# Performance work log

Hardware: AMD Instinct MI355X
Metric: run time of the kernel (lower is better)

## Reference

```python
import jax, jax.numpy as jnp
import numpy as np

D_MODEL, D_K, D_V, NUM_HEADS = 1024, 64, 64, 16
B, T = 4, 2048


def setup_inputs() -> dict:
    key = jax.random.key(0)
    ks = jax.random.split(key, 9)
    s = 0.02
    inp = {
        "input_Q": jax.random.normal(ks[0], (B, T, D_MODEL), dtype=jnp.float32),
        # causal mask: True = masked out (matches torch masked_fill semantics)
        "mask": jnp.triu(jnp.ones((T, T), dtype=bool), k=1),
        "Wq": jax.random.normal(ks[1], (D_MODEL, D_K * NUM_HEADS), dtype=jnp.float32) * s,
        "bq": jnp.zeros((D_K * NUM_HEADS,), dtype=jnp.float32),
        "Wk": jax.random.normal(ks[2], (D_MODEL, D_K * NUM_HEADS), dtype=jnp.float32) * s,
        "bk": jnp.zeros((D_K * NUM_HEADS,), dtype=jnp.float32),
        "Wv": jax.random.normal(ks[3], (D_MODEL, D_V * NUM_HEADS), dtype=jnp.float32) * s,
        "bv": jnp.zeros((D_V * NUM_HEADS,), dtype=jnp.float32),
        "Wo": jax.random.normal(ks[4], (D_V * NUM_HEADS, D_MODEL), dtype=jnp.float32) * s,
        "bo": jnp.zeros((D_MODEL,), dtype=jnp.float32),
    }
    return inp


def reference(input_Q, mask, Wq, bq, Wk, bk, Wv, bv, Wo, bo):
    b, t, _ = input_Q.shape
    h, dk, dv = NUM_HEADS, D_K, D_V
    # projections, then split heads: [b, t, h*d] -> [b, h, t, d]
    Q = (input_Q @ Wq + bq).reshape(b, t, h, dk).transpose(0, 2, 1, 3)
    K = (input_Q @ Wk + bk).reshape(b, t, h, dk).transpose(0, 2, 1, 3)
    V = (input_Q @ Wv + bv).reshape(b, t, h, dv).transpose(0, 2, 1, 3)
    # scaled dot-product attention with full [b, h, t, t] scores (as original)
    scores = jnp.einsum("bhqd,bhkd->bhqk", Q, K) * (1.0 / np.sqrt(dk).astype(np.float32))
    scores = jnp.where(mask, jnp.float32(-jnp.inf), scores)
    attn = jax.nn.softmax(scores, axis=-1)
    ctx = jnp.einsum("bhqk,bhkd->bhqd", attn, V)  # [b, h, t, dv]
    combined = ctx.transpose(0, 2, 1, 3).reshape(b, t, h * dv)
    return combined @ Wo + bo
```

## Files before the change

kernel.cpp:

```cpp
#include <hip/hip_runtime.h>
#include <hip/hip_bf16.h>
#include <stdint.h>

#define B_  4
#define T_  2048
#define H_  16
#define DH  64
#define DM  1024

typedef unsigned short u16;
typedef float  f32x4  __attribute__((ext_vector_type(4)));
typedef u16    u16x4  __attribute__((ext_vector_type(4)));
typedef __bf16 bf16x8 __attribute__((ext_vector_type(8)));
typedef bf16x8 __attribute__((may_alias, aligned(16))) bf16x8_a;
typedef u16x4  __attribute__((may_alias, aligned(8)))  u16x4_a;

__device__ __forceinline__ void gld16(void* lds, const void* g) {
  __builtin_amdgcn_global_load_lds((const __attribute__((address_space(1))) unsigned int*)g,
                                   (__attribute__((address_space(3))) unsigned int*)lds,
                                   16, 0, 0);
}
__device__ __forceinline__ u16 f2b(float f) {
  __bf16 h = (__bf16)f; return __builtin_bit_cast(unsigned short, h);
}

__global__ void prep(const float* __restrict__ X,
                     const float* __restrict__ Wq, const float* __restrict__ Wk,
                     const float* __restrict__ Wv, const float* __restrict__ Wo,
                     u16* __restrict__ Xb,
                     u16* __restrict__ WqT, u16* __restrict__ WkT,
                     u16* __restrict__ WvT, u16* __restrict__ WoT) {
  if (blockIdx.z == 4) {
    const int bi = blockIdx.y * 16 + blockIdx.x;
#pragma unroll
    for (int p = 0; p < 32; ++p) {
      const int i = bi * 32768 + p * 1024 + threadIdx.x * 4;
      const f32x4 v = *(const f32x4*)&X[i];
      u16x4 o;
      o.x = f2b(v.x); o.y = f2b(v.y); o.z = f2b(v.z); o.w = f2b(v.w);
      *(u16x4_a*)&Xb[i] = o;
    }
    return;
  }
  const float* in; u16* out;
  switch (blockIdx.z) {
    case 0: in = Wq; out = WqT; break;
    case 1: in = Wk; out = WkT; break;
    case 2: in = Wv; out = WvT; break;
    default: in = Wo; out = WoT; break;
  }
  __shared__ u16 t[64][65];
  const int bx = blockIdx.x * 64, by = blockIdx.y * 64;
  const int tx = threadIdx.x & 63, ty = threadIdx.x >> 6;
  for (int i = ty; i < 64; i += 4) t[i][tx] = f2b(in[(size_t)(by + i) * DM + bx + tx]);
  __syncthreads();
  for (int i = ty; i < 64; i += 4) out[(size_t)(bx + i) * DM + by + tx] = t[tx][i];
}

__device__ __forceinline__ void gemm_bt_128(
    const u16* __restrict__ A, const u16* __restrict__ BT,
    const float* __restrict__ bias, float oscale,
    u16* __restrict__ C, float* __restrict__ Cf, int mode)
{
  constexpr int K = 1024, N = 1024;
  __shared__ __attribute__((aligned(16))) u16 lAB[128 * 128];
  u16* lA = lAB;
  u16* lB = lAB + 128 * 64;
  const int tid  = threadIdx.x;
  const int lane = tid & 63;
  const int quad = lane >> 4, ln = lane & 15;
  const int ln7 = ln & 7;
  const int wave = tid >> 6;
  const int wm = wave >> 1, wn = wave & 1;
  const int m0 = blockIdx.y * 128, n0 = blockIdx.x * 128;

  const f32x4 fz = {0.f, 0.f, 0.f, 0.f};
  f32x4 acc[4][4];
#pragma unroll
  for (int i = 0; i < 4; i++)
#pragma unroll
    for (int j = 0; j < 4; j++) acc[i][j] = fz;

  for (int k0 = 0; k0 < K; k0 += 64) {
    __syncthreads();
#pragma unroll
    for (int p = 0; p < 4; ++p) {
      const int P = p * 256 + tid;
      const int row = P >> 3, c = (P & 7) ^ (row & 7);
      gld16(&lA[P * 8], &A [(size_t)(m0 + row) * K + k0 + c * 8]);
      gld16(&lB[P * 8], &BT[(size_t)(n0 + row) * K + k0 + c * 8]);
    }
    __syncthreads();
#pragma unroll
    for (int ks = 0; ks < 2; ++ks) {
      bf16x8 af[4], bf[4];
#pragma unroll
      for (int i = 0; i < 4; i++)
        af[i] = *(const bf16x8_a*)&lA[(wm * 64 + i * 16 + ln) * 64 + (((ks * 4 + quad) ^ ln7) << 3)];
#pragma unroll
      for (int j = 0; j < 4; j++)
        bf[j] = *(const bf16x8_a*)&lB[(wn * 64 + j * 16 + ln) * 64 + (((ks * 4 + quad) ^ ln7) << 3)];
#pragma unroll
      for (int i = 0; i < 4; i++)
#pragma unroll
        for (int j = 0; j < 4; j++)
          acc[i][j] = __builtin_amdgcn_mfma_f32_16x16x32_bf16(af[i], bf[j], acc[i][j], 0, 0, 0);
    }
  }

  if (mode == 1) {
    __syncthreads();
#pragma unroll
    for (int j = 0; j < 4; j++) {
      const int nl = wn * 64 + j * 16 + ln;
      const float bn = bias[n0 + nl];
#pragma unroll
      for (int i = 0; i < 4; i++) {
        const int ml = wm * 64 + i * 16 + quad * 4;
        u16x4 o;
#pragma unroll
        for (int r = 0; r < 4; r++) o[r] = f2b((acc[i][j][r] + bn) * oscale);
        const int sc = (ml >> 3) ^ (nl & 15);
        *(u16x4_a*)&lAB[nl * 128 + sc * 8 + (ml & 7)] = o;
      }
    }
    __syncthreads();
    const int bb = m0 >> 11, t0 = m0 & 2047;
#pragma unroll
    for (int it = 0; it < 8; ++it) {
      const int P = it * 256 + tid;
      const int nl = P >> 4, c = P & 15;
      const bf16x8 v = *(const bf16x8_a*)&lAB[nl * 128 + ((c ^ (nl & 15)) << 3)];
      const int n = n0 + nl, h = n >> 6, d = n & 63;
      *(bf16x8_a*)&C[((size_t)((bb * H_ + h) * DH + d)) * T_ + t0 + c * 8] = v;
    }
    return;
  }

#pragma unroll
  for (int j = 0; j < 4; j++) {
    const int n = n0 + wn * 64 + j * 16 + ln;
    const float bn = bias[n];
#pragma unroll
    for (int i = 0; i < 4; i++) {
      const int mb = m0 + wm * 64 + i * 16 + quad * 4;
#pragma unroll
      for (int r = 0; r < 4; r++) {
        const int m = mb + r;
        const float v = (acc[i][j][r] + bn) * oscale;
        if (mode == 0) {
          const int b = m >> 11, t = m & 2047, h = n >> 6, d = n & 63;
          C[((size_t)((b * H_ + h) * T_ + t)) * DH + d] = f2b(v);
        } else {
          Cf[(size_t)m * N + n] = v;
        }
      }
    }
  }
}

__global__ __launch_bounds__(256, 2) void qkv_gemm(
    const u16* __restrict__ X,
    const u16* __restrict__ WqT, const u16* __restrict__ WkT, const u16* __restrict__ WvT,
    const float* __restrict__ bq, const float* __restrict__ bk, const float* __restrict__ bv,
    u16* __restrict__ Qo, u16* __restrict__ Ko, u16* __restrict__ Vto)
{
  const u16 *BT; const float* bias; u16* C; float sc; int mode;
  if (blockIdx.z == 0)      { BT = WqT; bias = bq; C = Qo;  sc = 0.1803368801111144f; mode = 0; }
  else if (blockIdx.z == 1) { BT = WkT; bias = bk; C = Ko;  sc = 1.0f;                mode = 0; }
  else                      { BT = WvT; bias = bv; C = Vto; sc = 1.0f;                mode = 1; }
  gemm_bt_128(X, BT, bias, sc, C, nullptr, mode);
}

__global__ __launch_bounds__(256, 2) void out_gemm(
    const u16* __restrict__ ctx, const u16* __restrict__ WoT,
    const float* __restrict__ bo, float* __restrict__ out)
{
  gemm_bt_128(ctx, WoT, bo, 1.0f, nullptr, out, 2);
}

__global__ __launch_bounds__(512, 4) void flash_attn(
    const u16* __restrict__ Q, const u16* __restrict__ Kg,
    const u16* __restrict__ Vt, u16* __restrict__ ctx)
{
  __shared__ __attribute__((aligned(16))) u16 lK[2][128 * 64];
  __shared__ __attribute__((aligned(16))) u16 lV[2][64 * 128];
  __shared__ __attribute__((aligned(16))) u16 lP[128 * 64];

  const int bh = blockIdx.x;
  const int b  = bh >> 4, h = bh & 15;
  const int qi = 15 - blockIdx.y;
  const int q0 = qi * 128;
  const int tid = threadIdx.x;
  const int lane = tid & 63, wave = tid >> 6;
  const int quad = lane >> 4, ln = lane & 15;
  const int ln7 = ln & 7, ln8 = ln >> 3;
  const int w16 = wave * 16;

  const u16* Qbh = Q  + (size_t)bh * T_ * DH;
  const u16* Kbh = Kg + (size_t)bh * T_ * DH;
  const u16* Vbh = Vt + (size_t)bh * DH * T_;

  auto stage_kv = [&](int kt, int bufw) {
    const int t0 = kt << 7;
    u16* dK = lK[bufw]; u16* dV = lV[bufw];
#pragma unroll
    for (int p = 0; p < 2; ++p) {
      const int P = p * 512 + tid;
      const int row = P >> 3, c = (P & 7) ^ (row & 7);
      gld16(&dK[P * 8], &Kbh[(size_t)(t0 + row) * DH + c * 8]);
    }
#pragma unroll
    for (int p = 0; p < 2; ++p) {
      const int P = p * 512 + tid;
      const int row = P >> 4, c = (P & 15) ^ (row & 15);
      gld16(&dV[P * 8], &Vbh[(size_t)row * T_ + t0 + c * 8]);
    }
  };

#pragma unroll
  for (int p = 0; p < 2; ++p) {
    const int P = p * 512 + tid;
    const int row = P >> 3, c = (P & 7) ^ (row & 7);
    gld16(&lP[P * 8], &Qbh[(size_t)(q0 + row) * DH + c * 8]);
  }
  stage_kv(0, 0);
  asm volatile("s_waitcnt vmcnt(4)" ::: "memory");
  __builtin_amdgcn_s_barrier();
  bf16x8 aq[2];
#pragma unroll
  for (int ks = 0; ks < 2; ++ks)
    aq[ks] = *(const bf16x8_a*)&lP[(w16 + ln) * 64 + (((ks * 4 + quad) ^ ln7) << 3)];

  bf16x8 ones;
#pragma unroll
  for (int i = 0; i < 8; i++) ones[i] = (__bf16)1.0f;

  const f32x4 fz = {0.f, 0.f, 0.f, 0.f};
  f32x4 accO[4];
  f32x4 accL;
#pragma unroll
  for (int j = 0; j < 4; j++) accO[j] = fz;
  accL = fz;

  auto compute_tile = [&](int kt, const u16* lKb, const u16* lVb, bool MASK) {
    const int t0 = kt * 128;
#pragma unroll
    for (int half = 0; half < 2; ++half) {
      f32x4 s[4];
#pragma unroll
      for (int jj = 0; jj < 4; jj++) s[jj] = fz;
      __builtin_amdgcn_s_setprio(1);
#pragma unroll
      for (int ks = 0; ks < 2; ++ks) {
        bf16x8 bk4[4];
#pragma unroll
        for (int jj = 0; jj < 4; jj++)
          bk4[jj] = *(const bf16x8_a*)&lKb[((half * 4 + jj) * 16 + ln) * 64 + (((ks * 4 + quad) ^ ln7) << 3)];
#pragma unroll
        for (int jj = 0; jj < 4; jj++)
          s[jj] = __builtin_amdgcn_mfma_f32_16x16x32_bf16(aq[ks], bk4[jj], s[jj], 0, 0, 0);
      }
      __builtin_amdgcn_s_setprio(0);

#pragma unroll
      for (int jj = 0; jj < 4; jj++)
#pragma unroll
        for (int r = 0; r < 4; r++) {
          float z = s[jj][r];
          if (MASK) {
            const int qrow = q0 + w16 + quad * 4 + r;
            if ((t0 + (half * 4 + jj) * 16 + ln) > qrow) z = -INFINITY;
          }
          s[jj][r] = __builtin_amdgcn_exp2f(z);
        }

#pragma unroll
      for (int jj = 0; jj < 4; jj++) {
        const int c = jj * 2 + ln8;
#pragma unroll
        for (int r = 0; r < 4; r++) {
          const int row = w16 + quad * 4 + r;
          lP[row * 64 + ((c ^ (row & 7)) << 3) + ln7] = f2b(s[jj][r]);
        }
      }

#pragma unroll
      for (int ks2 = 0; ks2 < 2; ++ks2) {
        const int ks = half * 2 + ks2;
        bf16x8 ap, bv4[4];
        ap = *(const bf16x8_a*)&lP[(w16 + ln) * 64 + (((ks2 * 4 + quad) ^ ln7) << 3)];
#pragma unroll
        for (int j2 = 0; j2 < 4; j2++)
          bv4[j2] = *(const bf16x8_a*)&lVb[(j2 * 16 + ln) * 128 + (((ks * 4 + quad) ^ ln) << 3)];
        __builtin_amdgcn_s_setprio(1);
        accL = __builtin_amdgcn_mfma_f32_16x16x32_bf16(ap, ones, accL, 0, 0, 0);
#pragma unroll
        for (int j2 = 0; j2 < 4; j2++)
          accO[j2] = __builtin_amdgcn_mfma_f32_16x16x32_bf16(ap, bv4[j2], accO[j2], 0, 0, 0);
        __builtin_amdgcn_s_setprio(0);
      }
    }
  };

  int buf = 0;
  for (int kt = 0; kt < qi; ++kt) {
    __builtin_amdgcn_s_barrier();
    stage_kv(kt + 1, buf ^ 1);
    asm volatile("s_waitcnt vmcnt(4)" ::: "memory");
    __builtin_amdgcn_s_barrier();
    compute_tile(kt, lK[buf], lV[buf], false);
    buf ^= 1;
  }
  __builtin_amdgcn_s_barrier();
  asm volatile("s_waitcnt vmcnt(0)" ::: "memory");
  __builtin_amdgcn_s_barrier();
  compute_tile(qi, lK[buf], lV[buf], true);

#pragma unroll
  for (int r = 0; r < 4; r++) {
    const int qrow = q0 + w16 + quad * 4 + r;
    const float inv = 1.0f / accL[r];
#pragma unroll
    for (int j2 = 0; j2 < 4; j2++) {
      const int d = j2 * 16 + ln;
      ctx[((size_t)(b * T_ + qrow)) * DM + h * DH + d] = f2b(accO[j2][r] * inv);
    }
  }
}

extern "C" void kernel_launch(void* const* d_in, const int* in_sizes, int n_in,
                              void* d_out, int out_size, void* d_ws, size_t ws_size,
                              hipStream_t stream) {
  (void)in_sizes; (void)n_in; (void)out_size; (void)ws_size;
  const float* X  = (const float*)d_in[0];
  const float* Wq = (const float*)d_in[2];
  const float* bq = (const float*)d_in[3];
  const float* Wk = (const float*)d_in[4];
  const float* bk = (const float*)d_in[5];
  const float* Wv = (const float*)d_in[6];
  const float* bv = (const float*)d_in[7];
  const float* Wo = (const float*)d_in[8];
  const float* bo = (const float*)d_in[9];
  float* out = (float*)d_out;

  char* ws = (char*)d_ws;
  u16* WqT = (u16*)(ws + (0ull  << 20));
  u16* WkT = (u16*)(ws + (2ull  << 20));
  u16* WvT = (u16*)(ws + (4ull  << 20));
  u16* WoT = (u16*)(ws + (6ull  << 20));
  u16* Xb  = (u16*)(ws + (8ull  << 20));
  u16* Qb  = (u16*)(ws + (24ull << 20));
  u16* Kb  = (u16*)(ws + (40ull << 20));
  u16* Vtb = (u16*)(ws + (72ull << 20));
  u16* ctx = (u16*)(ws + (88ull << 20));

  prep<<<dim3(16, 16, 5), 256, 0, stream>>>(X, Wq, Wk, Wv, Wo, Xb, WqT, WkT, WvT, WoT);
  qkv_gemm<<<dim3(8, 64, 3), 256, 0, stream>>>(Xb, WqT, WkT, WvT, bq, bk, bv, Qb, Kb, Vtb);
  flash_attn<<<dim3(64, 16), 512, 0, stream>>>(Qb, Kb, Vtb, ctx);
  out_gemm<<<dim3(8, 64), 256, 0, stream>>>(ctx, WoT, bo, out);
}
```

Measured before the change: 275.4 us.

## Stage GEMM epilogues through LDS for coalesced stores and swizzle block order

The Q/K projection epilogue now writes bf16 results into a swizzled LDS tile and then issues 16-byte coalesced stores to the head-major layout, replacing scattered 2-byte global writes. The fp32 output GEMM epilogue likewise stages half-tiles through LDS and emits 16-byte row-contiguous stores. Both GEMMs switch to a 1D grid with a remapped block order, so that blocks running at the same time are spread across the XCDs. The costs are extra LDS traffic and barriers in the epilogues.

After: 251.7 us. -8.6%, faster.

```diff
diff --git a/kernel.cpp b/kernel.cpp
--- a/kernel.cpp
+++ b/kernel.cpp
@@ -14,6 +14,7 @@
 typedef __bf16 bf16x8 __attribute__((ext_vector_type(8)));
 typedef bf16x8 __attribute__((may_alias, aligned(16))) bf16x8_a;
 typedef u16x4  __attribute__((may_alias, aligned(8)))  u16x4_a;
+typedef f32x4  __attribute__((may_alias, aligned(16))) f32x4_a;
 
 __device__ __forceinline__ void gld16(void* lds, const void* g) {
   __builtin_amdgcn_global_load_lds((const __attribute__((address_space(1))) unsigned int*)g,
@@ -60,7 +61,8 @@
 __device__ __forceinline__ void gemm_bt_128(
     const u16* __restrict__ A, const u16* __restrict__ BT,
     const float* __restrict__ bias, float oscale,
-    u16* __restrict__ C, float* __restrict__ Cf, int mode)
+    u16* __restrict__ C, float* __restrict__ Cf, int mode,
+    int m0, int n0)
 {
   constexpr int K = 1024, N = 1024;
   __shared__ __attribute__((aligned(16))) u16 lAB[128 * 128];
@@ -72,7 +74,6 @@
   const int ln7 = ln & 7;
   const int wave = tid >> 6;
   const int wm = wave >> 1, wn = wave & 1;
-  const int m0 = blockIdx.y * 128, n0 = blockIdx.x * 128;
 
   const f32x4 fz = {0.f, 0.f, 0.f, 0.f};
   f32x4 acc[4][4];
@@ -106,6 +107,36 @@
         for (int j = 0; j < 4; j++)
           acc[i][j] = __builtin_amdgcn_mfma_f32_16x16x32_bf16(af[i], bf[j], acc[i][j], 0, 0, 0);
     }
+  }
+
+  if (mode == 0) {
+    __syncthreads();
+#pragma unroll
+    for (int j = 0; j < 4; j++) {
+      const int nl = wn * 64 + j * 16 + ln;
+      const float bn = bias[n0 + nl];
+      const int cc = nl >> 3, wic = nl & 7;
+#pragma unroll
+      for (int i = 0; i < 4; i++) {
+#pragma unroll
+        for (int r = 0; r < 4; r++) {
+          const int ml = wm * 64 + i * 16 + quad * 4 + r;
+          lAB[ml * 128 + ((cc ^ ((ml >> 2) & 7)) << 3) + wic] =
+              f2b((acc[i][j][r] + bn) * oscale);
+        }
+      }
+    }
+    __syncthreads();
+    const int bb = m0 >> 11, t0 = m0 & 2047, h0 = n0 >> 6;
+#pragma unroll
+    for (int it = 0; it < 8; ++it) {
+      const int P = it * 256 + tid;
+      const int ml = P >> 4, cc = P & 15;
+      const bf16x8 v = *(const bf16x8_a*)&lAB[ml * 128 + ((cc ^ ((ml >> 2) & 7)) << 3)];
+      const int h = h0 + (cc >> 3), d = (cc & 7) * 8;
+      *(bf16x8_a*)&C[((size_t)((bb * H_ + h) * T_ + t0 + ml)) * DH + d] = v;
+    }
+    return;
   }
 
   if (mode == 1) {
@@ -137,25 +168,35 @@
     return;
   }
 
-#pragma unroll
-  for (int j = 0; j < 4; j++) {
-    const int n = n0 + wn * 64 + j * 16 + ln;
-    const float bn = bias[n];
-#pragma unroll
-    for (int i = 0; i < 4; i++) {
-      const int mb = m0 + wm * 64 + i * 16 + quad * 4;
-#pragma unroll
-      for (int r = 0; r < 4; r++) {
-        const int m = mb + r;
-        const float v = (acc[i][j][r] + bn) * oscale;
-        if (mode == 0) {
-          const int b = m >> 11, t = m & 2047, h = n >> 6, d = n & 63;
-          C[((size_t)((b * H_ + h) * T_ + t)) * DH + d] = f2b(v);
-        } else {
-          Cf[(size_t)m * N + n] = v;
+  float* lF = (float*)lAB;
+  __syncthreads();
+#pragma unroll
+  for (int h2 = 0; h2 < 2; ++h2) {
+#pragma unroll
+    for (int ii = 0; ii < 2; ++ii) {
+      const int i = h2 * 2 + ii;
+#pragma unroll
+      for (int j = 0; j < 4; j++) {
+        const int nl = wn * 64 + j * 16 + ln;
+        const float bn = bias[n0 + nl];
+        const int cf = nl >> 2, wic = nl & 3;
+#pragma unroll
+        for (int r = 0; r < 4; r++) {
+          const int lr = wm * 32 + ii * 16 + quad * 4 + r;
+          lF[lr * 128 + ((cf ^ ((lr >> 2) & 7)) << 2) + wic] = acc[i][j][r] + bn;
         }
       }
     }
+    __syncthreads();
+#pragma unroll
+    for (int it = 0; it < 8; ++it) {
+      const int P = it * 256 + tid;
+      const int lr = P >> 5, cf = P & 31;
+      const f32x4 v = *(const f32x4_a*)&lF[lr * 128 + ((cf ^ ((lr >> 2) & 7)) << 2)];
+      const int ml = (lr >> 5) * 64 + h2 * 32 + (lr & 31);
+      *(f32x4_a*)&Cf[(size_t)(m0 + ml) * N + n0 + cf * 4] = v;
+    }
+    __syncthreads();
   }
 }
 
@@ -165,18 +206,25 @@
     const float* __restrict__ bq, const float* __restrict__ bk, const float* __restrict__ bv,
     u16* __restrict__ Qo, u16* __restrict__ Ko, u16* __restrict__ Vto)
 {
+  const int raw = blockIdx.x;
+  const int swz = (raw & 7) * 192 + (raw >> 3);
+  const int z = swz >> 9, r2 = swz & 511;
+  const int m0 = (r2 >> 3) * 128, n0 = (r2 & 7) * 128;
   const u16 *BT; const float* bias; u16* C; float sc; int mode;
-  if (blockIdx.z == 0)      { BT = WqT; bias = bq; C = Qo;  sc = 0.1803368801111144f; mode = 0; }
-  else if (blockIdx.z == 1) { BT = WkT; bias = bk; C = Ko;  sc = 1.0f;                mode = 0; }
-  else                      { BT = WvT; bias = bv; C = Vto; sc = 1.0f;                mode = 1; }
-  gemm_bt_128(X, BT, bias, sc, C, nullptr, mode);
+  if (z == 0)      { BT = WqT; bias = bq; C = Qo;  sc = 0.1803368801111144f; mode = 0; }
+  else if (z == 1) { BT = WkT; bias = bk; C = Ko;  sc = 1.0f;                mode = 0; }
+  else             { BT = WvT; bias = bv; C = Vto; sc = 1.0f;                mode = 1; }
+  gemm_bt_128(X, BT, bias, sc, C, nullptr, mode, m0, n0);
 }
 
 __global__ __launch_bounds__(256, 2) void out_gemm(
     const u16* __restrict__ ctx, const u16* __restrict__ WoT,
     const float* __restrict__ bo, float* __restrict__ out)
 {
-  gemm_bt_128(ctx, WoT, bo, 1.0f, nullptr, out, 2);
+  const int raw = blockIdx.x;
+  const int swz = (raw & 7) * 64 + (raw >> 3);
+  const int m0 = (swz >> 3) * 128, n0 = (swz & 7) * 128;
+  gemm_bt_128(ctx, WoT, bo, 1.0f, nullptr, out, 2, m0, n0);
 }
 
 __global__ __launch_bounds__(512, 4) void flash_attn(
@@ -356,7 +404,7 @@
   u16* ctx = (u16*)(ws + (88ull << 20));
 
   prep<<<dim3(16, 16, 5), 256, 0, stream>>>(X, Wq, Wk, Wv, Wo, Xb, WqT, WkT, WvT, WoT);
-  qkv_gemm<<<dim3(8, 64, 3), 256, 0, stream>>>(Xb, WqT, WkT, WvT, bq, bk, bv, Qb, Kb, Vtb);
+  qkv_gemm<<<dim3(1536), 256, 0, stream>>>(Xb, WqT, WkT, WvT, bq, bk, bv, Qb, Kb, Vtb);
   flash_attn<<<dim3(64, 16), 512, 0, stream>>>(Qb, Kb, Vtb, ctx);
-  out_gemm<<<dim3(8, 64), 256, 0, stream>>>(ctx, WoT, bo, out);
-}
+  out_gemm<<<dim3(512), 256, 0, stream>>>(ctx, WoT, bo, out);
+}
```
